# Performance work log

Measured on AMD Instinct MI355X. Metric: run time of the kernel, lower is better.

The kernel has to match this reference:

```python
import jax, jax.numpy as jnp
import numpy as np

DIM = 512
TEMB_DIM = 512
NUM_HEADS = 16
WS = 16  # window_size
N = WS * WS
B = 256


def _relative_position_index(ws: int) -> np.ndarray:
    """Swin-style relative position index, shape [ws*ws, ws*ws], values in [0, (2ws-1)^2)."""
    coords = np.stack(np.meshgrid(np.arange(ws), np.arange(ws), indexing='ij'))  # [2, ws, ws]
    flat = coords.reshape(2, -1)                                                  # [2, N]
    rel = flat[:, :, None] - flat[:, None, :]                                     # [2, N, N]
    rel = rel.transpose(1, 2, 0).copy()                                           # [N, N, 2]
    rel[:, :, 0] += ws - 1
    rel[:, :, 1] += ws - 1
    rel[:, :, 0] *= 2 * ws - 1
    return rel.sum(-1).astype(np.int32)


def setup_inputs() -> dict:
    key = jax.random.key(0)
    ks = jax.random.split(key, 8)
    lin = lambda k, fan_in, shape: jax.random.normal(k, shape, jnp.float32) * (1.0 / np.sqrt(fan_in))
    return {
        'x': jax.random.normal(ks[0], (B, N, DIM), jnp.float32),
        'temb': jax.random.normal(ks[1], (B, TEMB_DIM), jnp.float32),
        'qkv_w': lin(ks[2], DIM, (DIM, 3 * DIM)),
        'qkv_b': jnp.zeros((3 * DIM,), jnp.float32),
        'temb_w': lin(ks[3], TEMB_DIM, (TEMB_DIM, 3 * DIM)),
        'temb_b': jnp.zeros((3 * DIM,), jnp.float32),
        'rpb_table': jax.random.normal(ks[4], ((2 * WS - 1) ** 2, NUM_HEADS), jnp.float32) * 0.02,
        'proj_w': lin(ks[5], DIM, (DIM, DIM)),
        'proj_b': jnp.zeros((DIM,), jnp.float32),
        'rp_index': jnp.asarray(_relative_position_index(WS)),
    }


def reference(x, temb, qkv_w, qkv_b, temb_w, temb_b, rpb_table, proj_w, proj_b, rp_index):
    Bq, Nq, C = x.shape
    H = NUM_HEADS
    hd = C // H
    # qkv with time-embedding modulation: [B, N, 3C]
    qkv = x @ qkv_w + qkv_b + (temb @ temb_w + temb_b)[:, None, :]
    qkv = qkv.reshape(Bq, Nq, 3, H, hd).transpose(2, 0, 3, 1, 4)  # [3, B, H, N, hd]
    q, k, v = qkv[0], qkv[1], qkv[2]
    # relative position bias: [H, N, N]
    bias = rpb_table[rp_index.reshape(-1)].reshape(Nq, Nq, H).transpose(2, 0, 1)
    scale = 1.0 / jnp.sqrt(jnp.asarray(hd, x.dtype))  # SDPA default scale
    scores = jnp.einsum('bhqd,bhkd->bhqk', q, k) * scale + bias[None]
    attn = jax.nn.softmax(scores, axis=-1)
    out = jnp.einsum('bhqk,bhkd->bhqd', attn, v)       # [B, H, N, hd]
    out = out.transpose(0, 2, 1, 3).reshape(Bq, Nq, C)
    return out @ proj_w + proj_b
```

## Files before the change

kernel.cpp:

```cpp
#include <hip/hip_runtime.h>
#include <hip/hip_bf16.h>

#define B_ 256
#define N_ 256
#define H_ 16
#define SCALE2_ 0.25504526484f
#define LOG2E_ 1.4426950408889634f

typedef __attribute__((ext_vector_type(8))) short short8;
typedef __attribute__((ext_vector_type(4))) float f32x4v;
typedef unsigned int u32;

#define GLOAD16(gptr, lptr)                                                        \
  __builtin_amdgcn_global_load_lds((const __attribute__((address_space(1))) u32*)(gptr), \
                                   (__attribute__((address_space(3))) u32*)(lptr), 16, 0, 0)

static __device__ __forceinline__ unsigned cvt_pk_bf16(float lo, float hi) {
  unsigned r;
  asm("v_cvt_pk_bf16_f32 %0, %1, %2" : "=v"(r) : "v"(lo), "v"(hi));
  return r;
}

__global__ __launch_bounds__(512)
void prep_kernel(const float* __restrict__ temb, const float* __restrict__ temb_w,
                 const float* __restrict__ temb_b, const float* __restrict__ qkv_b,
                 float* __restrict__ tm,
                 const float* __restrict__ x, unsigned* __restrict__ xb16,
                 const float* __restrict__ qkv_w, unsigned short* __restrict__ qkv_wT,
                 const float* __restrict__ proj_w, unsigned short* __restrict__ proj_wT) {
  __shared__ __align__(16) char lbuf[17024];
  const int blk = blockIdx.x;
  const int t = threadIdx.x;

  if (blk < 256) {
    float* ts = (float*)lbuf;
    const int b = blk;
    ts[t] = temb[(size_t)b * 512 + t];
    __syncthreads();
    float a0 = temb_b[t] + qkv_b[t];
    float a1 = temb_b[t + 512] + qkv_b[t + 512];
    float a2 = temb_b[t + 1024] + qkv_b[t + 1024];
#pragma unroll 8
    for (int k = 0; k < 512; ++k) {
      const float tv = ts[k];
      const float* wr = temb_w + (size_t)k * 1536 + t;
      a0 += tv * wr[0];
      a1 += tv * wr[512];
      a2 += tv * wr[1024];
    }
    float* o = tm + (size_t)b * 1536 + t;
    o[0] = a0; o[512] = a1; o[1024] = a2;
  } else if (blk < 1280) {
    const int n8 = (B_ * N_ * 512) / 8;
    int i = (blk - 256) * 512 + t;
    for (; i < n8; i += 1024 * 512) {
      const float4* p = reinterpret_cast<const float4*>(x + (size_t)i * 8);
      float4 a = p[0], b4 = p[1];
      uint4 vv = make_uint4(cvt_pk_bf16(a.x, a.y), cvt_pk_bf16(a.z, a.w),
                            cvt_pk_bf16(b4.x, b4.y), cvt_pk_bf16(b4.z, b4.w));
      *reinterpret_cast<uint4*>(xb16 + (size_t)i * 4) = vv;
    }
  } else {
    const float* src; unsigned short* dst; int ncols, k0, n0;
    if (blk < 1472) {
      const int idx = blk - 1280;
      src = qkv_w; dst = qkv_wT; ncols = 1536;
      k0 = (idx / 12) << 5; n0 = (idx % 12) << 7;
    } else {
      const int idx = blk - 1472;
      src = proj_w; dst = proj_wT; ncols = 512;
      k0 = (idx >> 2) << 5; n0 = (idx & 3) << 7;
    }
    float (*tile)[133] = (float (*)[133])lbuf;
    {
      const int kk = t >> 4, c0 = (t & 15) << 3;
      const float* s = src + (size_t)(k0 + kk) * ncols + n0 + c0;
      float4 v0 = *reinterpret_cast<const float4*>(s);
      float4 v1 = *reinterpret_cast<const float4*>(s + 4);
      tile[kk][c0 + 0] = v0.x; tile[kk][c0 + 1] = v0.y; tile[kk][c0 + 2] = v0.z; tile[kk][c0 + 3] = v0.w;
      tile[kk][c0 + 4] = v1.x; tile[kk][c0 + 5] = v1.y; tile[kk][c0 + 6] = v1.z; tile[kk][c0 + 7] = v1.w;
    }
    __syncthreads();
    {
      const int nn = t >> 2, ck = (t & 3) << 3;
      uint4 vv = make_uint4(cvt_pk_bf16(tile[ck + 0][nn], tile[ck + 1][nn]),
                            cvt_pk_bf16(tile[ck + 2][nn], tile[ck + 3][nn]),
                            cvt_pk_bf16(tile[ck + 4][nn], tile[ck + 5][nn]),
                            cvt_pk_bf16(tile[ck + 6][nn], tile[ck + 7][nn]));
      *reinterpret_cast<uint4*>(dst + (size_t)(n0 + nn) * 512 + k0 + ck) = vv;
    }
  }
}

__global__ __launch_bounds__(512, 4)
void fused_attn_kernel(const unsigned short* __restrict__ xb16,
                       const unsigned short* __restrict__ wT,
                       const float* __restrict__ rpb,
                       const float* __restrict__ tm,
                       unsigned short* __restrict__ attn_out) {
  __shared__ __align__(16) char smem[67584];
  short* xs     = (short*)smem;
  short* ksp    = (short*)(smem + 16384);
  short* vTs    = (short*)(smem + 32768);
  short* wstage = (short*)(smem + 49152);
  float* biasT  = (float*)(smem + 49152);

  const int u = blockIdx.x;
  const int bh = ((u & 7) << 9) | (u >> 3);
  const int b = bh >> 4, h = bh & 15;
  const int tid = threadIdx.x;
  const int w = tid >> 6, l = tid & 63;
  const int l16 = l & 15, g = l >> 4;
  const int gsw8 = (g ^ ((l16 >> 1) & 3)) << 3;
  const int lrow = l >> 2;
  const int lcol = (((l & 3) ^ ((l >> 3) & 3)) << 3);

  const unsigned short* xsrc0 = xb16 + (size_t)(b * 256 + w * 16 + lrow) * 512 + lcol;
  const unsigned short* xsrc1 = xsrc0 + (size_t)128 * 512;
  const int row96 = w * 16 + lrow;
  const unsigned short* wsrc = wT + (size_t)((row96 >> 5) * 512 + h * 32 + (row96 & 31)) * 512 + lcol;

  f32x4v acc[2][6];
#pragma unroll
  for (int mt = 0; mt < 2; ++mt)
#pragma unroll
    for (int nt = 0; nt < 6; ++nt) acc[mt][nt] = (f32x4v)(0.0f);

  auto stage = [&](int t, int bufi) {
    const int k0 = t << 5;
    GLOAD16(xsrc0 + k0, xs + bufi * 8192 + w * 512);
    GLOAD16(xsrc1 + k0, xs + bufi * 8192 + (8 + w) * 512);
    if (w < 6) GLOAD16(wsrc + k0, wstage + bufi * 3072 + w * 512);
  };
  stage(0, 0);
#pragma unroll
  for (int t = 0; t < 16; ++t) {
    const int buf = t % 3;
    if (t < 15) {
      stage(t + 1, (t + 1) % 3);
      if (w < 6) asm volatile("s_waitcnt vmcnt(3)" ::: "memory");
      else       asm volatile("s_waitcnt vmcnt(2)" ::: "memory");
    } else {
      asm volatile("s_waitcnt vmcnt(0)" ::: "memory");
    }
    __builtin_amdgcn_sched_barrier(0);
    __builtin_amdgcn_s_barrier();
    __builtin_amdgcn_sched_barrier(0);
    short* xb = xs + buf * 8192;
    short* wb = wstage + buf * 3072;
    short8 af[2], bfr[6];
#pragma unroll
    for (int mt = 0; mt < 2; ++mt)
      af[mt] = *reinterpret_cast<short8*>(&xb[(w * 32 + mt * 16 + l16) * 32 + gsw8]);
#pragma unroll
    for (int nt = 0; nt < 6; ++nt)
      bfr[nt] = *reinterpret_cast<short8*>(&wb[(nt * 16 + l16) * 32 + gsw8]);
#pragma unroll
    for (int mt = 0; mt < 2; ++mt)
#pragma unroll
      for (int nt = 0; nt < 6; ++nt)
        acc[mt][nt] = __builtin_amdgcn_mfma_f32_16x16x32_bf16(af[mt], bfr[nt], acc[mt][nt], 0, 0, 0);
  }
  __syncthreads();

  const float* tmb = tm + (size_t)b * 1536 + h * 32;
#pragma unroll
  for (int nt = 0; nt < 6; ++nt) {
    const int prt = nt >> 1;
    const int d = ((nt & 1) << 4) + l16;
    const float tmv = tmb[(prt << 9) + d];
#pragma unroll
    for (int mt = 0; mt < 2; ++mt) {
      const int r0 = w * 32 + mt * 16 + g * 4;
      float v0 = acc[mt][nt][0] + tmv, v1 = acc[mt][nt][1] + tmv;
      float v2 = acc[mt][nt][2] + tmv, v3 = acc[mt][nt][3] + tmv;
      if (prt == 0) { v0 *= SCALE2_; v1 *= SCALE2_; v2 *= SCALE2_; v3 *= SCALE2_; }
      const u32 p01 = cvt_pk_bf16(v0, v1);
      const u32 p23 = cvt_pk_bf16(v2, v3);
      if (prt != 2) {
        short* dst = (prt == 0) ? xs : ksp;
        const int unit01 = ((d >> 3) ^ ((r0 >> 1) & 3)) << 3;
        const int base = r0 * 32 + unit01 + (d & 7);
        dst[base]            = (short)p01;
        dst[base + 32]       = (short)(p01 >> 16);
        dst[(base + 64) ^ 8] = (short)p23;
        dst[(base + 96) ^ 8] = (short)(p23 >> 16);
      } else {
#pragma unroll
        for (int j = 0; j < 4; ++j) {
          const int key = r0 + j;
          const int vcol = ((key >> 5) << 5) | (((key & 15) << 1) | ((key >> 4) & 1));
          const int unit = ((vcol >> 3) ^ (d & 7));
          const u32 pk = (j < 2) ? p01 : p23;
          vTs[d * 256 + (unit << 3) + (vcol & 7)] = (short)(pk >> ((j & 1) << 4));
        }
      }
    }
  }
  for (int e = tid; e < 961; e += 512) biasT[e] = rpb[e * 16 + h] * LOG2E_;
  __syncthreads();

  short8 bq[2];
#pragma unroll
  for (int mt = 0; mt < 2; ++mt)
    bq[mt] = *reinterpret_cast<short8*>(&xs[(w * 32 + mt * 16 + l16) * 32 + gsw8]);

  const int bcol = l16 - (g << 2) + 15;
  const int brow0 = w * 2 + 15;

  f32x4v bp_prev;
#pragma unroll
  for (int j = 0; j < 4; ++j) bp_prev[j] = biasT[(brow0 + 1) * 31 + bcol - j];

  short8 ones8;
#pragma unroll
  for (int j = 0; j < 8; ++j) ones8[j] = (short)0x3F80;

  f32x4v oacc[2][2];
  f32x4v oaccL[2];
#pragma unroll
  for (int mt = 0; mt < 2; ++mt) {
    oacc[mt][0] = (f32x4v)(0.0f);
    oacc[mt][1] = (f32x4v)(0.0f);
    oaccL[mt] = (f32x4v)(0.0f);
  }

#pragma unroll
  for (int kc = 0; kc < 8; ++kc) {
    const int kt0 = kc * 2, kt1 = kc * 2 + 1;
    short8 kf0 = *reinterpret_cast<short8*>(&ksp[(kt0 * 16 + l16) * 32 + gsw8]);
    short8 kf1 = *reinterpret_cast<short8*>(&ksp[(kt1 * 16 + l16) * 32 + gsw8]);
    f32x4v cA, cB;
    const float* brA = biasT + (brow0 - kt0) * 31 + bcol;
    const float* brB = biasT + (brow0 - kt1) * 31 + bcol;
#pragma unroll
    for (int j = 0; j < 4; ++j) { cA[j] = brA[-j]; cB[j] = brB[-j]; }
    f32x4v s00, s01, s10, s11;
    __builtin_amdgcn_s_setprio(1);
    s00 = __builtin_amdgcn_mfma_f32_16x16x32_bf16(kf0, bq[0], cA, 0, 0, 0);
    s01 = __builtin_amdgcn_mfma_f32_16x16x32_bf16(kf0, bq[1], bp_prev, 0, 0, 0);
    s10 = __builtin_amdgcn_mfma_f32_16x16x32_bf16(kf1, bq[0], cB, 0, 0, 0);
    s11 = __builtin_amdgcn_mfma_f32_16x16x32_bf16(kf1, bq[1], cA, 0, 0, 0);
    __builtin_amdgcn_s_setprio(0);
    bp_prev = cB;

    short8 pa0, pa1;
    {
      union { u32 u[4]; short8 s8; } pk0, pk1;
#pragma unroll
      for (int j = 0; j < 4; ++j) {
        pk0.u[j] = cvt_pk_bf16(exp2f(s00[j]), exp2f(s10[j]));
        pk1.u[j] = cvt_pk_bf16(exp2f(s01[j]), exp2f(s11[j]));
      }
      pa0 = pk0.s8; pa1 = pk1.s8;
    }
    short8 bv0 = *reinterpret_cast<short8*>(
        &vTs[(l16) * 256 + ((((kc * 4 + g) ^ (l16 & 7)) << 3))]);
    short8 bv1 = *reinterpret_cast<short8*>(
        &vTs[(16 + l16) * 256 + ((((kc * 4 + g) ^ (l16 & 7)) << 3))]);
    __builtin_amdgcn_s_setprio(1);
    oacc[0][0] = __builtin_amdgcn_mfma_f32_16x16x32_bf16(pa0, bv0, oacc[0][0], 0, 0, 0);
    oacc[0][1] = __builtin_amdgcn_mfma_f32_16x16x32_bf16(pa0, bv1, oacc[0][1], 0, 0, 0);
    oacc[1][0] = __builtin_amdgcn_mfma_f32_16x16x32_bf16(pa1, bv0, oacc[1][0], 0, 0, 0);
    oacc[1][1] = __builtin_amdgcn_mfma_f32_16x16x32_bf16(pa1, bv1, oacc[1][1], 0, 0, 0);
    oaccL[0]   = __builtin_amdgcn_mfma_f32_16x16x32_bf16(pa0, ones8, oaccL[0], 0, 0, 0);
    oaccL[1]   = __builtin_amdgcn_mfma_f32_16x16x32_bf16(pa1, ones8, oaccL[1], 0, 0, 0);
    __builtin_amdgcn_s_setprio(0);
  }

  float i0[4], i1[4];
#pragma unroll
  for (int j = 0; j < 4; ++j) {
    i0[j] = __builtin_amdgcn_rcpf(oaccL[0][j]);
    i1[j] = __builtin_amdgcn_rcpf(oaccL[1][j]);
  }
  short* ob = xs + w * 1024;
  const int u0 = (((l16 >> 3) ^ g) << 3) + (l16 & 7);
  const int u1 = ((((l16 >> 3) | 2) ^ g) << 3) + (l16 & 7);
  {
    const u32 a01 = cvt_pk_bf16(oacc[0][0][0] * i0[0], oacc[0][0][1] * i0[1]);
    const u32 a23 = cvt_pk_bf16(oacc[0][0][2] * i0[2], oacc[0][0][3] * i0[3]);
    const u32 b01 = cvt_pk_bf16(oacc[0][1][0] * i0[0], oacc[0][1][1] * i0[1]);
    const u32 b23 = cvt_pk_bf16(oacc[0][1][2] * i0[2], oacc[0][1][3] * i0[3]);
    const u32 c01 = cvt_pk_bf16(oacc[1][0][0] * i1[0], oacc[1][0][1] * i1[1]);
    const u32 c23 = cvt_pk_bf16(oacc[1][0][2] * i1[2], oacc[1][0][3] * i1[3]);
    const u32 d01 = cvt_pk_bf16(oacc[1][1][0] * i1[0], oacc[1][1][1] * i1[1]);
    const u32 d23 = cvt_pk_bf16(oacc[1][1][2] * i1[2], oacc[1][1][3] * i1[3]);
    const int r0 = (g << 2) * 32;
    ob[r0 + u0]       = (short)a01;  ob[r0 + 32 + u0]  = (short)(a01 >> 16);
    ob[r0 + 64 + u0]  = (short)a23;  ob[r0 + 96 + u0]  = (short)(a23 >> 16);
    ob[r0 + u1]       = (short)b01;  ob[r0 + 32 + u1]  = (short)(b01 >> 16);
    ob[r0 + 64 + u1]  = (short)b23;  ob[r0 + 96 + u1]  = (short)(b23 >> 16);
    const int r1 = r0 + 512;
    ob[r1 + u0]       = (short)c01;  ob[r1 + 32 + u0]  = (short)(c01 >> 16);
    ob[r1 + 64 + u0]  = (short)c23;  ob[r1 + 96 + u0]  = (short)(c23 >> 16);
    ob[r1 + u1]       = (short)d01;  ob[r1 + 32 + u1]  = (short)(d01 >> 16);
    ob[r1 + 64 + u1]  = (short)d23;  ob[r1 + 96 + u1]  = (short)(d23 >> 16);
  }
  unsigned short* aw = attn_out + (size_t)(b * 256 + w * 32) * 512 + h * 32;
#pragma unroll
  for (int i = 0; i < 2; ++i) {
    const int r = i * 16 + (l >> 2);
    const int cu = l & 3;
    const int su = cu ^ ((r >> 2) & 3);
    short8 vv = *reinterpret_cast<short8*>(&ob[r * 32 + (su << 3)]);
    *reinterpret_cast<short8*>(aw + (size_t)r * 512 + (cu << 3)) = vv;
  }
}

__global__ __launch_bounds__(256)
void proj_kernel(const unsigned short* __restrict__ A,
                 const unsigned short* __restrict__ BT,
                 const float* __restrict__ proj_b,
                 float* __restrict__ out) {
  __shared__ short As[2][4096];
  __shared__ short Bs[2][4096];
  const int bid0 = blockIdx.x;
  const int swz = ((bid0 & 7) << 8) | (bid0 >> 3);
  const int m0 = (swz >> 2) << 7;
  const int n0 = (swz & 3) << 7;
  const int tid = threadIdx.x;
  const int w = tid >> 6, l = tid & 63, l16 = l & 15, g = l >> 4;
  const int wr = w >> 1, wc = w & 1;
  const int gsw8 = (g ^ ((l16 >> 1) & 3)) << 3;
  const int lrow = l >> 2;
  const int lcol = (((l & 3) ^ ((l >> 3) & 3)) << 3);

  const unsigned short* asrc0 = A + (size_t)(m0 + w * 16 + lrow) * 512 + lcol;
  const unsigned short* asrc1 = asrc0 + (size_t)64 * 512;
  const unsigned short* bsrc0 = BT + (size_t)(n0 + w * 16 + lrow) * 512 + lcol;
  const unsigned short* bsrc1 = bsrc0 + (size_t)64 * 512;

  f32x4v acc[4][4];
#pragma unroll
  for (int mt = 0; mt < 4; ++mt)
#pragma unroll
    for (int nt = 0; nt < 4; ++nt) acc[mt][nt] = (f32x4v)(0.0f);

  auto stage = [&](int t, int bufi) {
    const int k0 = t << 5;
    GLOAD16(asrc0 + k0, As[bufi] + w * 512);
    GLOAD16(asrc1 + k0, As[bufi] + (4 + w) * 512);
    GLOAD16(bsrc0 + k0, Bs[bufi] + w * 512);
    GLOAD16(bsrc1 + k0, Bs[bufi] + (4 + w) * 512);
  };
  stage(0, 0);
#pragma unroll
  for (int t = 0; t < 16; ++t) {
    asm volatile("s_waitcnt vmcnt(0)" ::: "memory");
    __builtin_amdgcn_sched_barrier(0);
    __builtin_amdgcn_s_barrier();
    __builtin_amdgcn_sched_barrier(0);
    if (t < 15) stage(t + 1, (t + 1) & 1);
    const int cur = t & 1;
    short8 af[4], bfr[4];
#pragma unroll
    for (int mt = 0; mt < 4; ++mt)
      af[mt] = *reinterpret_cast<short8*>(&As[cur][(wr * 64 + mt * 16 + l16) * 32 + gsw8]);
#pragma unroll
    for (int nt = 0; nt < 4; ++nt)
      bfr[nt] = *reinterpret_cast<short8*>(&Bs[cur][(wc * 64 + nt * 16 + l16) * 32 + gsw8]);
#pragma unroll
    for (int mt = 0; mt < 4; ++mt)
#pragma unroll
      for (int nt = 0; nt < 4; ++nt)
        acc[mt][nt] = __builtin_amdgcn_mfma_f32_16x16x32_bf16(af[mt], bfr[nt], acc[mt][nt], 0, 0, 0);
  }
#pragma unroll
  for (int nt = 0; nt < 4; ++nt) {
    const int col = n0 + wc * 64 + nt * 16 + l16;
    const float pb = proj_b[col];
#pragma unroll
    for (int mt = 0; mt < 4; ++mt)
#pragma unroll
      for (int j = 0; j < 4; ++j)
        out[(size_t)(m0 + wr * 64 + mt * 16 + g * 4 + j) * 512 + col] = acc[mt][nt][j] + pb;
  }
}

extern "C" void kernel_launch(void* const* d_in, const int* in_sizes, int n_in,
                              void* d_out, int out_size, void* d_ws, size_t ws_size,
                              hipStream_t stream) {
  const float* x      = (const float*)d_in[0];
  const float* temb   = (const float*)d_in[1];
  const float* qkv_w  = (const float*)d_in[2];
  const float* qkv_b  = (const float*)d_in[3];
  const float* temb_w = (const float*)d_in[4];
  const float* temb_b = (const float*)d_in[5];
  const float* rpb    = (const float*)d_in[6];
  const float* proj_w = (const float*)d_in[7];
  const float* proj_b = (const float*)d_in[8];
  float* out = (float*)d_out;

  char* ws = (char*)d_ws;
  float* tm               = (float*)ws;
  unsigned short* xb16    = (unsigned short*)(ws + 1572864);
  unsigned short* qkv_wT  = (unsigned short*)(ws + 1572864 + 67108864);
  unsigned short* proj_wT = (unsigned short*)(ws + 1572864 + 67108864 + 1572864);
  unsigned short* attn_ws = (unsigned short*)(ws + 1572864 + 67108864 + 1572864 + 524288);

  prep_kernel<<<1536, 512, 0, stream>>>(temb, temb_w, temb_b, qkv_b, tm,
                                        x, (unsigned*)xb16,
                                        qkv_w, qkv_wT, proj_w, proj_wT);
  fused_attn_kernel<<<B_ * H_, 512, 0, stream>>>(xb16, qkv_wT, rpb, tm, attn_ws);
  proj_kernel<<<2048, 256, 0, stream>>>(attn_ws, proj_wT, proj_b, out);
}
```

Baseline: 312.5 us.

## Load weight fragments directly from global and make x staging per-wave

```diff
diff --git a/kernel.cpp b/kernel.cpp
--- a/kernel.cpp
+++ b/kernel.cpp
@@ -98,12 +98,11 @@
                        const float* __restrict__ rpb,
                        const float* __restrict__ tm,
                        unsigned short* __restrict__ attn_out) {
-  __shared__ __align__(16) char smem[67584];
-  short* xs     = (short*)smem;
-  short* ksp    = (short*)(smem + 16384);
-  short* vTs    = (short*)(smem + 32768);
-  short* wstage = (short*)(smem + 49152);
-  float* biasT  = (float*)(smem + 49152);
+  __shared__ __align__(16) char smem[53008];
+  short* xs    = (short*)smem;
+  short* ksp   = (short*)(smem + 16384);
+  short* vTs   = (short*)(smem + 32768);
+  float* biasT = (float*)(smem + 49152);
 
   const int u = blockIdx.x;
   const int bh = ((u & 7) << 9) | (u >> 3);
@@ -115,10 +114,15 @@
   const int lrow = l >> 2;
   const int lcol = (((l & 3) ^ ((l >> 3) & 3)) << 3);
 
-  const unsigned short* xsrc0 = xb16 + (size_t)(b * 256 + w * 16 + lrow) * 512 + lcol;
-  const unsigned short* xsrc1 = xsrc0 + (size_t)128 * 512;
-  const int row96 = w * 16 + lrow;
-  const unsigned short* wsrc = wT + (size_t)((row96 >> 5) * 512 + h * 32 + (row96 & 31)) * 512 + lcol;
+  const unsigned short* xsrc0 = xb16 + (size_t)(b * 256 + w * 32 + lrow) * 512 + lcol;
+  const unsigned short* xsrc1 = xsrc0 + (size_t)16 * 512;
+
+  const unsigned short* wp[6];
+#pragma unroll
+  for (int nt = 0; nt < 6; ++nt) {
+    const int c = nt * 16 + l16;
+    wp[nt] = wT + (size_t)(((c >> 5) << 9) + h * 32 + (c & 31)) * 512 + g * 8;
+  }
 
   f32x4v acc[2][6];
 #pragma unroll
@@ -126,42 +130,37 @@
 #pragma unroll
     for (int nt = 0; nt < 6; ++nt) acc[mt][nt] = (f32x4v)(0.0f);
 
-  auto stage = [&](int t, int bufi) {
+  auto stage_x = [&](int t, int bufi) {
     const int k0 = t << 5;
-    GLOAD16(xsrc0 + k0, xs + bufi * 8192 + w * 512);
-    GLOAD16(xsrc1 + k0, xs + bufi * 8192 + (8 + w) * 512);
-    if (w < 6) GLOAD16(wsrc + k0, wstage + bufi * 3072 + w * 512);
+    GLOAD16(xsrc0 + k0, xs + bufi * 8192 + (2 * w) * 512);
+    GLOAD16(xsrc1 + k0, xs + bufi * 8192 + (2 * w + 1) * 512);
   };
-  stage(0, 0);
+  stage_x(0, 0);
 #pragma unroll
   for (int t = 0; t < 16; ++t) {
-    const int buf = t % 3;
+    const int k0 = t << 5;
+    short8 bfr[6];
+#pragma unroll
+    for (int nt = 0; nt < 6; ++nt)
+      bfr[nt] = *reinterpret_cast<const short8*>(wp[nt] + k0);
     if (t < 15) {
-      stage(t + 1, (t + 1) % 3);
-      if (w < 6) asm volatile("s_waitcnt vmcnt(3)" ::: "memory");
-      else       asm volatile("s_waitcnt vmcnt(2)" ::: "memory");
+      stage_x(t + 1, (t + 1) & 1);
+      asm volatile("s_waitcnt vmcnt(8)" ::: "memory");
     } else {
-      asm volatile("s_waitcnt vmcnt(0)" ::: "memory");
+      asm volatile("s_waitcnt vmcnt(6)" ::: "memory");
     }
     __builtin_amdgcn_sched_barrier(0);
-    __builtin_amdgcn_s_barrier();
-    __builtin_amdgcn_sched_barrier(0);
-    short* xb = xs + buf * 8192;
-    short* wb = wstage + buf * 3072;
-    short8 af[2], bfr[6];
+    short* xb = xs + (t & 1) * 8192;
+    short8 af[2];
 #pragma unroll
     for (int mt = 0; mt < 2; ++mt)
       af[mt] = *reinterpret_cast<short8*>(&xb[(w * 32 + mt * 16 + l16) * 32 + gsw8]);
 #pragma unroll
-    for (int nt = 0; nt < 6; ++nt)
-      bfr[nt] = *reinterpret_cast<short8*>(&wb[(nt * 16 + l16) * 32 + gsw8]);
-#pragma unroll
     for (int mt = 0; mt < 2; ++mt)
 #pragma unroll
       for (int nt = 0; nt < 6; ++nt)
         acc[mt][nt] = __builtin_amdgcn_mfma_f32_16x16x32_bf16(af[mt], bfr[nt], acc[mt][nt], 0, 0, 0);
   }
-  __syncthreads();
 
   const float* tmb = tm + (size_t)b * 1536 + h * 32;
 #pragma unroll
```

Result: slower. 509.4 us (+63.0%).
